# Performance work log

Hardware: AMD Instinct MI355X
Metric: run time of the kernel (lower is better)

## Reference

```python
import jax, jax.numpy as jnp
import numpy as np

N_LAYERS = 8
DILATIONS = [1, 2, 1, 2, 1, 2, 1, 2]
K_HOPS = 3
BN = 13248   # batch(64) * n_nodes(207), merged as in the torch module
L = 13       # 12 history steps + 1; shrinks by sum(dilations)=12 across layers
E = 211968   # BN * avg_degree(16)


def _conv1d(x, w, b, dil):
    # x: (BN, Cin, L), w: (Cout, Cin, 2) kernel-2 dilated conv, VALID (causal shrink)
    y = jax.lax.conv_general_dilated(x, w, (1,), 'VALID', rhs_dilation=(dil,),
                                     dimension_numbers=('NCH', 'OIH', 'NCH'))
    return y + b[None, :, None]


def setup_inputs() -> dict:
    key = jax.random.key(0)
    ks = jax.random.split(key, 20)
    s = 0.1  # keep activations in a sane range
    return {
        'x': jax.random.normal(ks[0], (BN, L, 2), jnp.float32),
        'edge_src': jax.random.randint(ks[1], (E,), 0, BN),
        'edge_dst': jax.random.randint(ks[2], (E,), 0, BN),
        'edge_w': jax.random.uniform(ks[3], (E,), jnp.float32),
        'init_w': s * jax.random.normal(ks[4], (2, 32), jnp.float32),
        'init_b': s * jax.random.normal(ks[5], (32,), jnp.float32),
        'filt_w': s * jax.random.normal(ks[6], (8, 32, 32, 2), jnp.float32),
        'filt_b': s * jax.random.normal(ks[7], (8, 32), jnp.float32),
        'gate_w': s * jax.random.normal(ks[8], (8, 32, 32, 2), jnp.float32),
        'gate_b': s * jax.random.normal(ks[9], (8, 32), jnp.float32),
        'gcn_w': s * jax.random.normal(ks[10], (8, 6, 32, 32), jnp.float32),
        'gcn_b': s * jax.random.normal(ks[11], (8, 32), jnp.float32),
        'skip_w': s * jax.random.normal(ks[12], (8, 256, 32), jnp.float32),
        'skip_b': s * jax.random.normal(ks[13], (8, 256), jnp.float32),
        'out0_w': s * jax.random.normal(ks[14], (256, 512), jnp.float32),
        'out0_b': s * jax.random.normal(ks[15], (512,), jnp.float32),
        'out1_w': s * jax.random.normal(ks[16], (512, 12), jnp.float32),
        'out1_b': s * jax.random.normal(ks[17], (12,), jnp.float32),
    }


def reference(x, edge_src, edge_dst, edge_w, init_w, init_b,
              filt_w, filt_b, gate_w, gate_b, gcn_w, gcn_b,
              skip_w, skip_b, out0_w, out0_b, out1_w, out1_b):
    # init linear: (BN, L, 2) -> (BN, L, 32) -> (BN, 32, L)
    h = (x @ init_w + init_b).transpose(0, 2, 1)
    # per-hop edge weights: elementwise powers of the transition weights
    # (faithful to repo's dense_to_sparse(transition ** k)); bck = transposed edges
    adjs = [(edge_src, edge_dst, edge_w ** k) for k in range(1, K_HOPS + 1)] + \
           [(edge_dst, edge_src, edge_w ** k) for k in range(1, K_HOPS + 1)]
    skip = None
    for l in range(N_LAYERS):
        d = DILATIONS[l]
        res = h
        # Gated TCN: tanh(filter) * sigmoid(gate), seq shrinks by d
        t = jnp.tanh(_conv1d(h, filt_w[l], filt_b[l], d)) * \
            jax.nn.sigmoid(_conv1d(h, gate_w[l], gate_b[l], d))
        # Diffusion conv: sum over 6 adjacency types of A_w (x W_a)
        xt = t.transpose(0, 2, 1)  # (BN, L', 32)
        g = jnp.zeros_like(xt)
        for a, (src, dst, w) in enumerate(adjs):
            msg = (xt @ gcn_w[l, a])[src] * w[:, None, None]  # (E, L', 32)
            g = g + jax.ops.segment_sum(msg, dst, num_segments=BN)
        h = g.transpose(0, 2, 1) + gcn_b[l][None, :, None]  # (BN, 32, L')
        # residual connection (align shrunk sequence)
        h = h + res[:, :, -h.shape[-1]:]
        # skip conv (1x1) on last timestep, accumulated
        sc = h[:, :, -1] @ skip_w[l].T + skip_b[l]  # (BN, 256)
        skip = sc if skip is None else skip + sc
    out = jax.nn.relu(skip)
    out = jax.nn.relu(out @ out0_w + out0_b)
    return out @ out1_w + out1_b  # (BN, 12)
```

## Files before the change

### kernel.cpp

```cpp
#include <hip/hip_runtime.h>
#include <hip/hip_fp16.h>

#define BN 13248
#define NE 211968
#define NBKT 8
#define SCAN_TOT (BN * NBKT)
#define SCAN_NBLK 52
#define ZSTRIDE 200
#define HSTRIDE 40
#define HNODE 480

typedef __attribute__((ext_vector_type(8))) short bf16x8;
typedef __attribute__((ext_vector_type(8))) _Float16 f16x8;
typedef __attribute__((ext_vector_type(4))) float f32x4;

__device__ __forceinline__ f32x4 mfma16b(bf16x8 a, bf16x8 b, f32x4 c) {
  return __builtin_amdgcn_mfma_f32_16x16x32_bf16(a, b, c, 0, 0, 0);
}
__device__ __forceinline__ f32x4 mfma16h(f16x8 a, f16x8 b, f32x4 c) {
  return __builtin_amdgcn_mfma_f32_16x16x32_f16(a, b, c, 0, 0, 0);
}

__device__ __forceinline__ unsigned short to_bf16(float v) {
  unsigned bits = __float_as_uint(v);
  return (unsigned short)((bits + 0x7FFFu + ((bits >> 16) & 1u)) >> 16);
}
__device__ __forceinline__ unsigned short to_f16(float v) {
  union { __half h; unsigned short s; } u; u.h = __float2half(v); return u.s;
}
__device__ __forceinline__ unsigned h2u(__half2 h) {
  union { __half2 h; unsigned u; } v; v.h = h; return v.u;
}
__device__ __forceinline__ __half2 u2h(unsigned u) {
  union { unsigned u; __half2 h; } v; v.u = u; return v.h;
}

__device__ __forceinline__ float fast_tanh(float x) {
  float e2 = __expf(2.f * x);
  return 1.f - 2.f / (e2 + 1.f);
}
__device__ __forceinline__ float fast_sig(float x) {
  return 1.f / (1.f + __expf(-x));
}

__global__ void k_count(const int* __restrict__ src, const int* __restrict__ dst,
                        int* __restrict__ cur_f, int* __restrict__ cur_b) {
  int e = blockIdx.x * 256 + threadIdx.x;
  if (e < NE) {
    int s = src[e], t = dst[e];
    atomicAdd(&cur_f[t * NBKT + (s >> 11)], 1);
    atomicAdd(&cur_b[s * NBKT + (t >> 11)], 1);
  }
}

__global__ __launch_bounds__(1024) void k_scan1(int* __restrict__ cnt_f, int* __restrict__ cnt_b,
                                                int* __restrict__ bsum) {
  __shared__ int sdata[1024];
  int b = blockIdx.x;
  int dir = (b >= SCAN_NBLK) ? 1 : 0;
  int lb = dir ? b - SCAN_NBLK : b;
  int* cnt = dir ? cnt_b : cnt_f;
  int tid = threadIdx.x;
  int i0 = lb * 2048 + tid * 2;
  int v0 = (i0 < SCAN_TOT) ? cnt[i0] : 0;
  int v1 = (i0 + 1 < SCAN_TOT) ? cnt[i0 + 1] : 0;
  int tot = v0 + v1;
  sdata[tid] = tot;
  __syncthreads();
  for (int off = 1; off < 1024; off <<= 1) {
    int add = (tid >= off) ? sdata[tid - off] : 0;
    __syncthreads();
    sdata[tid] += add;
    __syncthreads();
  }
  int excl = sdata[tid] - tot;
  if (i0 < SCAN_TOT) cnt[i0] = excl;
  if (i0 + 1 < SCAN_TOT) cnt[i0 + 1] = excl + v0;
  if (tid == 1023) bsum[b] = sdata[1023];
}

__global__ void k_scan2(int* __restrict__ bsum) {
  __shared__ int sdata[128];
  int tid = threadIdx.x;
  int seg = (tid >= 64) ? 64 : 0;
  int src = (tid < 64) ? tid : tid - 64 + SCAN_NBLK;
  int valid = ((tid & 63) < SCAN_NBLK);
  int v = valid ? bsum[src] : 0;
  sdata[tid] = v;
  __syncthreads();
  for (int off = 1; off < 64; off <<= 1) {
    int add = (tid - off >= seg) ? sdata[tid - off] : 0;
    __syncthreads();
    sdata[tid] += add;
    __syncthreads();
  }
  if (valid) bsum[src] = sdata[tid] - v;
}

__global__ __launch_bounds__(1024) void k_scan3(int* __restrict__ cnt_f, int* __restrict__ cnt_b,
                                                const int* __restrict__ bsum,
                                                int* __restrict__ row_f, int* __restrict__ row_b) {
  int b = blockIdx.x;
  int dir = (b >= SCAN_NBLK) ? 1 : 0;
  int lb = dir ? b - SCAN_NBLK : b;
  int* cnt = dir ? cnt_b : cnt_f;
  int* row = dir ? row_b : row_f;
  int off = bsum[b];
  int tid = threadIdx.x;
#pragma unroll
  for (int k = 0; k < 2; ++k) {
    int idx = lb * 2048 + tid * 2 + k;
    if (idx < SCAN_TOT) {
      int v = cnt[idx] + off;
      cnt[idx] = v;
      if ((idx & (NBKT - 1)) == 0) row[idx / NBKT] = v;
    }
  }
  if (b == 0 && tid == 0) { row_f[BN] = NE; row_b[BN] = NE; }
}

__global__ void k_fill(const int* __restrict__ src, const int* __restrict__ dst,
                       const float* __restrict__ w,
                       int* __restrict__ cur_f, int4* __restrict__ ce_f,
                       int* __restrict__ cur_b, int4* __restrict__ ce_b) {
  int e = blockIdx.x * 256 + threadIdx.x;
  if (e < NE) {
    int s = src[e], t = dst[e];
    float wv = w[e];
    float w2 = wv * wv, w3 = w2 * wv;
    int u1 = (int)h2u(__float2half2_rn(wv));
    int u2 = (int)h2u(__float2half2_rn(w2));
    int u3 = (int)h2u(__float2half2_rn(w3));
    int p = atomicAdd(&cur_f[t * NBKT + (s >> 11)], 1); ce_f[p] = make_int4(s, u1, u2, u3);
    int q = atomicAdd(&cur_b[s * NBKT + (t >> 11)], 1); ce_b[q] = make_int4(t, u1, u2, u3);
  }
}

__global__ void k_init(const float* __restrict__ x, const float* __restrict__ iw,
                       const float* __restrict__ ib, float* __restrict__ h) {
  int idx = blockIdx.x * 256 + threadIdx.x;
  if (idx >= BN * 13 * 32) return;
  int c = idx & 31;
  int r = idx >> 5;
  int n = r % BN;
  int tau = r / BN;
  float x0 = x[(n * 13 + tau) * 2 + 0];
  float x1 = x[(n * 13 + tau) * 2 + 1];
  h[idx] = fmaf(x0, iw[c], fmaf(x1, iw[32 + c], ib[c]));
}

__global__ void k_pack(const float* __restrict__ skip_w, const float* __restrict__ skip_b,
                       const float* __restrict__ w0, const float* __restrict__ w1,
                       const float* __restrict__ gcn_w,
                       const float* __restrict__ filt_w, const float* __restrict__ gate_w,
                       unsigned short* __restrict__ SWb, unsigned short* __restrict__ W0T,
                       unsigned short* __restrict__ W1T, float* __restrict__ bsum,
                       unsigned short* __restrict__ Gg16, unsigned short* __restrict__ WTC) {
  int id = blockIdx.x * 256 + threadIdx.x;
  if (id < 65536) {
    int j = id >> 8, k = id & 255;
    SWb[id] = to_bf16(skip_w[((k >> 5) * 256 + j) * 32 + (k & 31)]);
  }
  if (id < 131072) {
    int jo = id >> 8, k = id & 255;
    W0T[id] = to_bf16(w0[k * 512 + jo]);
  }
  if (id < 8192) {
    int n = id >> 9, k = id & 511;
    W1T[id] = (n < 12) ? to_bf16(w1[k * 12 + n]) : (unsigned short)0;
  }
  if (id < 256) {
    float s = 0.f;
    for (int l = 0; l < 8; ++l) s += skip_b[l * 256 + id];
    bsum[id] = s;
  }
  if (id < 49152) {
    int l = id / 6144, rem = id % 6144;
    int co = rem / 192, k = rem % 192;
    int a = k >> 5, ci = k & 31;
    Gg16[id] = to_f16(gcn_w[((l * 6 + a) * 32 + ci) * 32 + co]);
  }
  if (id < 32768) {
    int l = id >> 12, rem = id & 4095;
    int g = rem >> 11, co = (rem >> 6) & 31, k = rem & 63;
    const float* srcw = (g ? gate_w : filt_w) + l * 2048;
    float v = (k < 32) ? srcw[(co * 32 + k) * 2 + 0] : srcw[(co * 32 + (k - 32)) * 2 + 1];
    WTC[id] = to_f16(v);
  }
}

template<int LIN, int D, int TPAD>
__global__ __launch_bounds__(256) void k_tcn(const float* __restrict__ h_in, unsigned short* __restrict__ t_out,
    const float* __restrict__ fw, const float* __restrict__ fb,
    const float* __restrict__ gw, const float* __restrict__ gb) {
  constexpr int LOUT = LIN - D;
  __shared__ __align__(16) float wq[32 * 32 * 4];
  __shared__ float hl[8][LIN * 32];
  int tid = threadIdx.x;
  for (int f = tid; f < 4096; f += 256) {
    int e = f & 3, co = (f >> 2) & 31, ci = f >> 7;
    const float* srcw = (e < 2) ? fw : gw;
    wq[f] = srcw[(co * 32 + ci) * 2 + (e & 1)];
  }
  int n0 = blockIdx.x * 8;
  for (int i = tid; i < 8 * LIN * 32; i += 256) {
    int c = i & 31, r = i >> 5;
    int nl = r / LIN, tau = r % LIN;
    hl[nl][tau * 32 + c] = h_in[(tau * BN + n0 + nl) * 32 + c];
  }
  __syncthreads();
  int nl = tid >> 5, co = tid & 31;
  int n = n0 + nl;
  float accf[LOUT], accg[LOUT];
  float fbv = fb[co], gbv = gb[co];
#pragma unroll
  for (int j = 0; j < LOUT; ++j) { accf[j] = fbv; accg[j] = gbv; }
#pragma unroll
  for (int ci = 0; ci < 32; ++ci) {
    float4 wv = *(const float4*)&wq[(ci * 32 + co) * 4];
    float xr[LIN];
#pragma unroll
    for (int t = 0; t < LIN; ++t) xr[t] = hl[nl][t * 32 + ci];
#pragma unroll
    for (int j = 0; j < LOUT; ++j) {
      accf[j] = fmaf(xr[j], wv.x, accf[j]);
      accf[j] = fmaf(xr[j + D], wv.y, accf[j]);
      accg[j] = fmaf(xr[j], wv.z, accg[j]);
      accg[j] = fmaf(xr[j + D], wv.w, accg[j]);
    }
  }
#pragma unroll
  for (int j = 0; j < TPAD; ++j) {
    unsigned short v = 0;
    if (j < LOUT) v = to_f16(fast_tanh(accf[j < LOUT ? j : 0]) * fast_sig(accg[j < LOUT ? j : 0]));
    t_out[(n * TPAD + j) * 32 + co] = v;
  }
}

template<int NT>
__device__ __forceinline__ void edge_fma3(const int4& c, const uint2 (&u)[NT], __half2* A) {
  __half2 wh0 = u2h((unsigned)c.y), wh1 = u2h((unsigned)c.z), wh2 = u2h((unsigned)c.w);
#pragma unroll
  for (int j = 0; j < NT; ++j) {
    __half2 v0 = u2h(u[j].x), v1 = u2h(u[j].y);
    A[(0 * NT + j) * 2 + 0] = __hfma2(wh0, v0, A[(0 * NT + j) * 2 + 0]);
    A[(0 * NT + j) * 2 + 1] = __hfma2(wh0, v1, A[(0 * NT + j) * 2 + 1]);
    A[(1 * NT + j) * 2 + 0] = __hfma2(wh1, v0, A[(1 * NT + j) * 2 + 0]);
    A[(1 * NT + j) * 2 + 1] = __hfma2(wh1, v1, A[(1 * NT + j) * 2 + 1]);
    A[(2 * NT + j) * 2 + 0] = __hfma2(wh2, v0, A[(2 * NT + j) * 2 + 0]);
    A[(2 * NT + j) * 2 + 1] = __hfma2(wh2, v1, A[(2 * NT + j) * 2 + 1]);
  }
}

template<int TPAD, int NT, int LOUTT>
__device__ __forceinline__ void gather_one(const unsigned short* __restrict__ t_in,
    int e0, int e1, const int4* __restrict__ ce, int rowoff0, int rowbase, __half2* A) {
  constexpr bool FULL = (LOUTT >= TPAD);
  constexpr int EB = (NT == 3) ? 3 : ((NT == 2) ? 4 : 6);
  int e = e0;
  for (; e + EB <= e1; e += EB) {
    int4 c[EB];
    uint2 u[EB][NT];
#pragma unroll
    for (int k = 0; k < EB; ++k) c[k] = ce[e + k];
#pragma unroll
    for (int k = 0; k < EB; ++k) {
      const unsigned short* p = t_in + c[k].x * (TPAD * 32) + rowoff0;
#pragma unroll
      for (int j = 0; j < NT; ++j)
        u[k][j] = (FULL || rowbase + j < LOUTT) ? *(const uint2*)(p + j * 32) : make_uint2(0u, 0u);
    }
    __builtin_amdgcn_sched_barrier(0);
#pragma unroll
    for (int k = 0; k < EB; ++k) edge_fma3<NT>(c[k], u[k], A);
  }
  for (; e < e1; ++e) {
    int4 c1 = ce[e];
    uint2 u1[NT];
    const unsigned short* p = t_in + c1.x * (TPAD * 32) + rowoff0;
#pragma unroll
    for (int j = 0; j < NT; ++j)
      u1[j] = (FULL || rowbase + j < LOUTT) ? *(const uint2*)(p + j * 32) : make_uint2(0u, 0u);
    edge_fma3<NT>(c1, u1, A);
  }
}

template<int LOUT, int D, int TPAD, int D2, int TPAD2, bool LAST>
__global__ __launch_bounds__(128, 8) void k_fused(
    const unsigned short* __restrict__ t_in,
    const float* __restrict__ h_in, float* __restrict__ h_out,
    float* __restrict__ lastcol, unsigned short* __restrict__ t_next,
    const int* __restrict__ row_f, const int4* __restrict__ ce_f,
    const int* __restrict__ row_b, const int4* __restrict__ ce_b,
    const unsigned short* __restrict__ Wg,
    const float* __restrict__ bias,
    const unsigned short* __restrict__ Wtc,
    const float* __restrict__ fbn, const float* __restrict__ gbn) {
  constexpr int NT = TPAD / 4;
  constexpr int LOUT2 = LAST ? 1 : (LOUT - D2);
  constexpr int ZROWS = (2 * TPAD + 15) & ~15;
  constexpr int SBYTES = ZROWS * ZSTRIDE * 2;
  __shared__ __align__(16) char smem[SBYTES];
  unsigned short* Zl = (unsigned short*)smem;
  unsigned short* hb16 = (unsigned short*)smem;
  int tid = threadIdx.x;
  int nl = tid >> 6;
  int lane = tid & 63;
  int dh = lane >> 5;
  int lane32 = lane & 31;
  int tl = lane32 >> 3;
  int c4 = (lane32 & 7) << 2;
  int n0 = blockIdx.x * 2;
  int n = n0 + nl;
  int rowbase = tl * NT;
  int rowoff0 = rowbase * 32 + c4;
  const int* rowp = dh ? row_b : row_f;
  const int4* ce  = dh ? ce_b : ce_f;
  int e0 = rowp[n], e1 = rowp[n + 1];
  __half2 acc[3 * NT * 2];
  __half2 zero = __float2half2_rn(0.f);
#pragma unroll
  for (int i = 0; i < 3 * NT * 2; ++i) acc[i] = zero;
  gather_one<TPAD, NT, LOUT>(t_in, e0, e1, ce, rowoff0, rowbase, acc);
#pragma unroll
  for (int j = 0; j < NT; ++j) {
    int m = nl * TPAD + rowbase + j;
#pragma unroll
    for (int a3 = 0; a3 < 3; ++a3) {
      uint2 v = make_uint2(h2u(acc[(a3 * NT + j) * 2 + 0]), h2u(acc[(a3 * NT + j) * 2 + 1]));
      *(uint2*)(&Zl[m * ZSTRIDE + (dh * 3 + a3) * 32 + c4]) = v;
    }
  }
  __syncthreads();
  int wave = nl;
  int m16 = lane & 15, q = lane >> 4;
  constexpr int UPW = ZROWS / 16;
  f32x4 dacc[UPW];
#pragma unroll
  for (int i = 0; i < UPW; ++i) {
    int u = wave * UPW + i;
    int mt = u >> 1, nt = u & 1;
    dacc[i] = (f32x4){0.f, 0.f, 0.f, 0.f};
#pragma unroll
    for (int ks = 0; ks < 6; ++ks) {
      f16x8 av = *(const f16x8*)(&Zl[(mt * 16 + m16) * ZSTRIDE + ks * 32 + q * 8]);
      f16x8 bv = *(const f16x8*)((const _Float16*)Wg + (nt * 16 + m16) * 192 + ks * 32 + q * 8);
      dacc[i] = mfma16h(av, bv, dacc[i]);
    }
  }
  __syncthreads();
#pragma unroll
  for (int i = 0; i < UPW; ++i) {
    int u = wave * UPW + i;
    int mt = u >> 1, nt = u & 1;
    int co = nt * 16 + m16;
    float bco = bias[co];
#pragma unroll
    for (int r = 0; r < 4; ++r) {
      int mm = mt * 16 + q * 4 + r;
      int node = mm / TPAD;
      int tau = mm % TPAD;
      if (mm < 2 * TPAD && tau < LOUT) {
        float rres = h_in[((tau + D) * BN + n0 + node) * 32 + co];
        float o = dacc[i][r] + bco + rres;
        h_out[(tau * BN + n0 + node) * 32 + co] = o;
        if (!LAST) hb16[node * HNODE + tau * HSTRIDE + co] = to_f16(o);
        if (tau == LOUT - 1) lastcol[(n0 + node) * 32 + co] = o;
      }
    }
  }
  if (!LAST) {
    __syncthreads();
#pragma unroll
    for (int i = 0; i < 2; ++i) {
      int u = wave * 2 + i;
      int node = u >> 1, ntc = u & 1;
      int co = ntc * 16 + m16;
      f32x4 df = (f32x4){0.f, 0.f, 0.f, 0.f};
      f32x4 dg = (f32x4){0.f, 0.f, 0.f, 0.f};
#pragma unroll
      for (int s = 0; s < 2; ++s) {
        f16x8 av = *(const f16x8*)(&hb16[node * HNODE + (m16 + s * D2) * HSTRIDE + q * 8]);
        f16x8 bvf = *(const f16x8*)((const _Float16*)Wtc + (0 * 32 + co) * 64 + s * 32 + q * 8);
        f16x8 bvg = *(const f16x8*)((const _Float16*)Wtc + (1 * 32 + co) * 64 + s * 32 + q * 8);
        df = mfma16h(av, bvf, df);
        dg = mfma16h(av, bvg, dg);
      }
      float fbv = fbn[co], gbv = gbn[co];
#pragma unroll
      for (int r = 0; r < 4; ++r) {
        int j = q * 4 + r;
        if (j < TPAD2) {
          unsigned short v = 0;
          if (j < LOUT2)
            v = to_f16(fast_tanh(df[r] + fbv) * fast_sig(dg[r] + gbv));
          t_next[((n0 + node) * TPAD2 + j) * 32 + co] = v;
        }
      }
    }
  }
}

__device__ __forceinline__ bf16x8 ldsA(const unsigned short* buf, int stride, int row, int ks, int q) {
  int unit = ks * 4 + q;
  int addr = row * stride + ((unit ^ (row & 7)) << 3);
  return *(const bf16x8*)(buf + addr);
}

__global__ __launch_bounds__(256) void k_final(const float* __restrict__ lastcol,
    const unsigned short* __restrict__ SWb, const unsigned short* __restrict__ W0T,
    const unsigned short* __restrict__ W1T, const float* __restrict__ bsum,
    const float* __restrict__ b0, const float* __restrict__ b1,
    float* __restrict__ out) {
  __shared__ __align__(16) unsigned short Z[32 * 256];
  __shared__ __align__(16) unsigned short H[32 * 512];
  int tid = threadIdx.x;
  int wave = tid >> 6, lane = tid & 63;
  int m16 = lane & 15, q = lane >> 4;
  int n0 = blockIdx.x * 32;
#pragma unroll
  for (int it = 0; it < 32; ++it) {
    int id = it * 256 + tid;
    int m = id >> 8, k = id & 255;
    float v = lastcol[((k >> 5) * BN + n0 + m) * 32 + (k & 31)];
    Z[m * 256 + (((k >> 3) ^ (m & 7)) << 3) + (k & 7)] = to_bf16(v);
  }
  __syncthreads();
  f32x4 acc1[2][4];
#pragma unroll
  for (int mt = 0; mt < 2; ++mt)
#pragma unroll
    for (int i = 0; i < 4; ++i) acc1[mt][i] = (f32x4){0.f, 0.f, 0.f, 0.f};
#pragma unroll
  for (int ks = 0; ks < 8; ++ks) {
    bf16x8 a0 = ldsA(Z, 256, m16, ks, q);
    bf16x8 a1 = ldsA(Z, 256, 16 + m16, ks, q);
#pragma unroll
    for (int i = 0; i < 4; ++i) {
      int j = (wave * 4 + i) * 16 + m16;
      bf16x8 b = *(const bf16x8*)(SWb + j * 256 + ks * 32 + q * 8);
      acc1[0][i] = mfma16b(a0, b, acc1[0][i]);
      acc1[1][i] = mfma16b(a1, b, acc1[1][i]);
    }
  }
  __syncthreads();
#pragma unroll
  for (int i = 0; i < 4; ++i) {
    int j = (wave * 4 + i) * 16 + m16;
    float bs = bsum[j];
#pragma unroll
    for (int mt = 0; mt < 2; ++mt)
#pragma unroll
      for (int r = 0; r < 4; ++r) {
        int row = mt * 16 + q * 4 + r;
        float v = fmaxf(acc1[mt][i][r] + bs, 0.f);
        Z[row * 256 + (((j >> 3) ^ (row & 7)) << 3) + (j & 7)] = to_bf16(v);
      }
  }
  __syncthreads();
  f32x4 acc2[2][8];
#pragma unroll
  for (int mt = 0; mt < 2; ++mt)
#pragma unroll
    for (int i = 0; i < 8; ++i) acc2[mt][i] = (f32x4){0.f, 0.f, 0.f, 0.f};
#pragma unroll
  for (int ks = 0; ks < 8; ++ks) {
    bf16x8 a0 = ldsA(Z, 256, m16, ks, q);
    bf16x8 a1 = ldsA(Z, 256, 16 + m16, ks, q);
#pragma unroll
    for (int i = 0; i < 8; ++i) {
      int jo = (wave * 8 + i) * 16 + m16;
      bf16x8 b = *(const bf16x8*)(W0T + jo * 256 + ks * 32 + q * 8);
      acc2[0][i] = mfma16b(a0, b, acc2[0][i]);
      acc2[1][i] = mfma16b(a1, b, acc2[1][i]);
    }
  }
#pragma unroll
  for (int i = 0; i < 8; ++i) {
    int jo = (wave * 8 + i) * 16 + m16;
    float b0v = b0[jo];
#pragma unroll
    for (int mt = 0; mt < 2; ++mt)
#pragma unroll
      for (int r = 0; r < 4; ++r) {
        int row = mt * 16 + q * 4 + r;
        float v = fmaxf(acc2[mt][i][r] + b0v, 0.f);
        H[row * 512 + (((jo >> 3) ^ (row & 7)) << 3) + (jo & 7)] = to_bf16(v);
      }
  }
  __syncthreads();
  if (wave < 2) {
    f32x4 acc3 = (f32x4){0.f, 0.f, 0.f, 0.f};
#pragma unroll
    for (int ks = 0; ks < 16; ++ks) {
      bf16x8 a = ldsA(H, 512, wave * 16 + m16, ks, q);
      bf16x8 b = *(const bf16x8*)(W1T + m16 * 512 + ks * 32 + q * 8);
      acc3 = mfma16b(a, b, acc3);
    }
    if (m16 < 12) {
      float bv = b1[m16];
#pragma unroll
      for (int r = 0; r < 4; ++r)
        out[(n0 + wave * 16 + q * 4 + r) * 12 + m16] = acc3[r] + bv;
    }
  }
}

extern "C" void kernel_launch(void* const* d_in, const int* in_sizes, int n_in,
                              void* d_out, int out_size, void* d_ws, size_t ws_size,
                              hipStream_t stream) {
  const float* x      = (const float*)d_in[0];
  const int*   esrc   = (const int*)d_in[1];
  const int*   edst   = (const int*)d_in[2];
  const float* ew     = (const float*)d_in[3];
  const float* init_w = (const float*)d_in[4];
  const float* init_b = (const float*)d_in[5];
  const float* filt_w = (const float*)d_in[6];
  const float* filt_b = (const float*)d_in[7];
  const float* gate_w = (const float*)d_in[8];
  const float* gate_b = (const float*)d_in[9];
  const float* gcn_w  = (const float*)d_in[10];
  const float* gcn_b  = (const float*)d_in[11];
  const float* skip_w = (const float*)d_in[12];
  const float* skip_b = (const float*)d_in[13];
  const float* w0     = (const float*)d_in[14];
  const float* b0     = (const float*)d_in[15];
  const float* w1     = (const float*)d_in[16];
  const float* b1     = (const float*)d_in[17];
  float* out = (float*)d_out;

  float* base = (float*)d_ws;
  float* hA      = base;
  float* hB      = hA + 13 * BN * 32;
  unsigned short* tA = (unsigned short*)(hB + 13 * BN * 32);
  unsigned short* tB = tA + 12 * BN * 32;
  float* lastcol = (float*)(tB + 12 * BN * 32);
  int* row_f = (int*)(lastcol + 8 * BN * 32);
  int* row_b = row_f + (BN + 2);
  int* bscan = row_b + (BN + 2);
  int* cur_f = bscan + 128;
  int* cur_b = cur_f + BN * NBKT;
  int4* ce_f = (int4*)(cur_b + BN * NBKT);
  int4* ce_b = ce_f + NE;
  unsigned short* SWb  = (unsigned short*)(ce_b + NE);
  unsigned short* W0T  = SWb + 65536;
  unsigned short* W1T  = W0T + 131072;
  unsigned short* Gg16 = W1T + 8192;
  unsigned short* WTC  = Gg16 + 49152;
  float* bsumv = (float*)(WTC + 32768);

  hipMemsetAsync(cur_f, 0, 2 * BN * NBKT * sizeof(int), stream);
  const int egrid = (NE + 255) / 256;
  k_count<<<egrid, 256, 0, stream>>>(esrc, edst, cur_f, cur_b);
  k_scan1<<<2 * SCAN_NBLK, 1024, 0, stream>>>(cur_f, cur_b, bscan);
  k_scan2<<<1, 128, 0, stream>>>(bscan);
  k_scan3<<<2 * SCAN_NBLK, 1024, 0, stream>>>(cur_f, cur_b, bscan, row_f, row_b);
  k_fill<<<egrid, 256, 0, stream>>>(esrc, edst, ew, cur_f, ce_f, cur_b, ce_b);
  k_init<<<(BN * 13 * 32 + 255) / 256, 256, 0, stream>>>(x, init_w, init_b, hA);
  k_pack<<<512, 256, 0, stream>>>(skip_w, skip_b, w0, w1, gcn_w, filt_w, gate_w,
                                  SWb, W0T, W1T, bsumv, Gg16, WTC);

  k_tcn<13, 1, 12><<<BN / 8, 256, 0, stream>>>(hA, tA, filt_w, filt_b, gate_w, gate_b);

#define FUSED(l, LOUTv, Dv, TPv, D2v, TP2v, LASTv, tin, tout, hin, hout) \
  k_fused<LOUTv, Dv, TPv, D2v, TP2v, LASTv><<<BN / 2, 128, 0, stream>>>( \
      tin, hin, hout, lastcol + l * BN * 32, tout, row_f, ce_f, row_b, ce_b, \
      Gg16 + l * 6144, gcn_b + l * 32, WTC + (l + 1) * 4096, \
      filt_b + (l + 1) * 32, gate_b + (l + 1) * 32);

  FUSED(0, 12, 1, 12, 2, 12, false, tA, tB, hA, hB)
  FUSED(1, 10, 2, 12, 1, 12, false, tB, tA, hB, hA)
  FUSED(2,  9, 1, 12, 2,  8, false, tA, tB, hA, hB)
  FUSED(3,  7, 2,  8, 1,  8, false, tB, tA, hB, hA)
  FUSED(4,  6, 1,  8, 2,  4, false, tA, tB, hA, hB)
  FUSED(5,  4, 2,  4, 1,  4, false, tB, tA, hB, hA)
  FUSED(6,  3, 1,  4, 2,  4, false, tA, tB, hA, hB)
#undef FUSED
  k_fused<1, 2, 4, 2, 4, true><<<BN / 2, 128, 0, stream>>>(
      tB, hB, hA, lastcol + 7 * BN * 32, tA, row_f, ce_f, row_b, ce_b,
      Gg16 + 7 * 6144, gcn_b + 7 * 32, WTC, filt_b, gate_b);

  k_final<<<BN / 32, 256, 0, stream>>>(lastcol, SWb, W0T, W1T, bsumv, b0, b1, out);
}
```

Before: 655.1 us.

## Restructure fused GCN gather into one-node-per-wave async LDS staging pipeline

The fused layer kernel now runs one 64-lane wave per node instead of two nodes per 128-thread block. Each edge's neighbour row is streamed into LDS with global_load_lds through an 8-deep ring buffer, paced by explicit vmcnt waits, and the edge lists are staged into LDS in chunks. Forward and backward directions are handled sequentially within the wave. The goal is to keep more gather loads in flight and avoid register-staged uint2 loads. The cost is more LDS use per block, serialised directions, hand-written waitcnt logic and a changed MFMA tiling to one 16-row tile per node.

```diff
diff --git a/kernel.cpp b/kernel.cpp
--- a/kernel.cpp
+++ b/kernel.cpp
@@ -8,7 +8,6 @@
 #define SCAN_NBLK 52
 #define ZSTRIDE 200
 #define HSTRIDE 40
-#define HNODE 480
 
 typedef __attribute__((ext_vector_type(8))) short bf16x8;
 typedef __attribute__((ext_vector_type(8))) _Float16 f16x8;
@@ -41,6 +40,48 @@
 }
 __device__ __forceinline__ float fast_sig(float x) {
   return 1.f / (1.f + __expf(-x));
+}
+
+template<int N>
+__device__ __forceinline__ void vmwait() {
+  if constexpr (N == 0)       asm volatile("s_waitcnt vmcnt(0)" ::: "memory");
+  else if constexpr (N == 7)  asm volatile("s_waitcnt vmcnt(7)" ::: "memory");
+  else if constexpr (N == 14) asm volatile("s_waitcnt vmcnt(14)" ::: "memory");
+  else if constexpr (N == 21) asm volatile("s_waitcnt vmcnt(21)" ::: "memory");
+  __builtin_amdgcn_sched_barrier(0);
+}
+
+template<int NJ>
+__device__ __forceinline__ void stage_edge(const unsigned short* t_in, int node,
+                                           char* stg, int slot, int lane) {
+  const char* g = (const char*)t_in + (size_t)node * (NJ * 256);
+  char* l = stg + slot * (NJ * 256);
+#pragma unroll
+  for (int j = 0; j < NJ; ++j)
+    __builtin_amdgcn_global_load_lds(
+        (const __attribute__((address_space(1))) void*)(g + j * 256 + lane * 4),
+        (__attribute__((address_space(3))) void*)(l + j * 256), 4, 0, 0);
+}
+
+__device__ __forceinline__ void stage_ce(const int4* ce, int4* celds, int g, int lane) {
+  __builtin_amdgcn_global_load_lds(
+      (const __attribute__((address_space(1))) void*)(ce + g * 64 + lane),
+      (__attribute__((address_space(3))) void*)(celds + g * 64), 16, 0, 0);
+}
+
+template<int NJ>
+__device__ __forceinline__ void consume_edge(const char* stg, int slot,
+                                             const int4* celds, int i, int lane, __half2* A) {
+  int4 cw = celds[i];
+  __half2 w1 = u2h((unsigned)cw.y), w2 = u2h((unsigned)cw.z), w3 = u2h((unsigned)cw.w);
+  const char* sp = stg + slot * (NJ * 256);
+#pragma unroll
+  for (int j = 0; j < NJ; ++j) {
+    __half2 v = *(const __half2*)(sp + (j * 64 + lane) * 4);
+    A[0 * NJ + j] = __hfma2(w1, v, A[0 * NJ + j]);
+    A[1 * NJ + j] = __hfma2(w2, v, A[1 * NJ + j]);
+    A[2 * NJ + j] = __hfma2(w3, v, A[2 * NJ + j]);
+  }
 }
 
 __global__ void k_count(const int* __restrict__ src, const int* __restrict__ dst,
@@ -237,56 +278,8 @@
   }
 }
 
-template<int NT>
-__device__ __forceinline__ void edge_fma3(const int4& c, const uint2 (&u)[NT], __half2* A) {
-  __half2 wh0 = u2h((unsigned)c.y), wh1 = u2h((unsigned)c.z), wh2 = u2h((unsigned)c.w);
-#pragma unroll
-  for (int j = 0; j < NT; ++j) {
-    __half2 v0 = u2h(u[j].x), v1 = u2h(u[j].y);
-    A[(0 * NT + j) * 2 + 0] = __hfma2(wh0, v0, A[(0 * NT + j) * 2 + 0]);
-    A[(0 * NT + j) * 2 + 1] = __hfma2(wh0, v1, A[(0 * NT + j) * 2 + 1]);
-    A[(1 * NT + j) * 2 + 0] = __hfma2(wh1, v0, A[(1 * NT + j) * 2 + 0]);
-    A[(1 * NT + j) * 2 + 1] = __hfma2(wh1, v1, A[(1 * NT + j) * 2 + 1]);
-    A[(2 * NT + j) * 2 + 0] = __hfma2(wh2, v0, A[(2 * NT + j) * 2 + 0]);
-    A[(2 * NT + j) * 2 + 1] = __hfma2(wh2, v1, A[(2 * NT + j) * 2 + 1]);
-  }
-}
-
-template<int TPAD, int NT, int LOUTT>
-__device__ __forceinline__ void gather_one(const unsigned short* __restrict__ t_in,
-    int e0, int e1, const int4* __restrict__ ce, int rowoff0, int rowbase, __half2* A) {
-  constexpr bool FULL = (LOUTT >= TPAD);
-  constexpr int EB = (NT == 3) ? 3 : ((NT == 2) ? 4 : 6);
-  int e = e0;
-  for (; e + EB <= e1; e += EB) {
-    int4 c[EB];
-    uint2 u[EB][NT];
-#pragma unroll
-    for (int k = 0; k < EB; ++k) c[k] = ce[e + k];
-#pragma unroll
-    for (int k = 0; k < EB; ++k) {
-      const unsigned short* p = t_in + c[k].x * (TPAD * 32) + rowoff0;
-#pragma unroll
-      for (int j = 0; j < NT; ++j)
-        u[k][j] = (FULL || rowbase + j < LOUTT) ? *(const uint2*)(p + j * 32) : make_uint2(0u, 0u);
-    }
-    __builtin_amdgcn_sched_barrier(0);
-#pragma unroll
-    for (int k = 0; k < EB; ++k) edge_fma3<NT>(c[k], u[k], A);
-  }
-  for (; e < e1; ++e) {
-    int4 c1 = ce[e];
-    uint2 u1[NT];
-    const unsigned short* p = t_in + c1.x * (TPAD * 32) + rowoff0;
-#pragma unroll
-    for (int j = 0; j < NT; ++j)
-      u1[j] = (FULL || rowbase + j < LOUTT) ? *(const uint2*)(p + j * 32) : make_uint2(0u, 0u);
-    edge_fma3<NT>(c1, u1, A);
-  }
-}
-
 template<int LOUT, int D, int TPAD, int D2, int TPAD2, bool LAST>
-__global__ __launch_bounds__(128, 8) void k_fused(
+__global__ __launch_bounds__(64, 6) void k_fused(
     const unsigned short* __restrict__ t_in,
     const float* __restrict__ h_in, float* __restrict__ h_out,
     float* __restrict__ lastcol, unsigned short* __restrict__ t_next,
@@ -296,76 +289,99 @@
     const float* __restrict__ bias,
     const unsigned short* __restrict__ Wtc,
     const float* __restrict__ fbn, const float* __restrict__ gbn) {
-  constexpr int NT = TPAD / 4;
+  constexpr int NJ = TPAD / 4;
   constexpr int LOUT2 = LAST ? 1 : (LOUT - D2);
-  constexpr int ZROWS = (2 * TPAD + 15) & ~15;
-  constexpr int SBYTES = ZROWS * ZSTRIDE * 2;
-  __shared__ __align__(16) char smem[SBYTES];
+  constexpr int Q = 8;
+  constexpr int CAP = 128;
+  constexpr int BLKB = NJ * 256;
+  constexpr int STAGEB = Q * BLKB;
+  constexpr int GATB = STAGEB + CAP * 16;
+  constexpr int ZB = 16 * ZSTRIDE * 2;
+  constexpr int SBYTES = GATB > ZB ? GATB : ZB;
+  __shared__ __align__(256) char smem[SBYTES];
+  char* stg = smem;
+  int4* celds = (int4*)(smem + STAGEB);
   unsigned short* Zl = (unsigned short*)smem;
   unsigned short* hb16 = (unsigned short*)smem;
-  int tid = threadIdx.x;
-  int nl = tid >> 6;
-  int lane = tid & 63;
-  int dh = lane >> 5;
-  int lane32 = lane & 31;
-  int tl = lane32 >> 3;
-  int c4 = (lane32 & 7) << 2;
-  int n0 = blockIdx.x * 2;
-  int n = n0 + nl;
-  int rowbase = tl * NT;
-  int rowoff0 = rowbase * 32 + c4;
-  const int* rowp = dh ? row_b : row_f;
-  const int4* ce  = dh ? ce_b : ce_f;
-  int e0 = rowp[n], e1 = rowp[n + 1];
-  __half2 acc[3 * NT * 2];
+  int lane = threadIdx.x;
+  int n = blockIdx.x;
+  __half2 acc[6 * NJ];
   __half2 zero = __float2half2_rn(0.f);
 #pragma unroll
-  for (int i = 0; i < 3 * NT * 2; ++i) acc[i] = zero;
-  gather_one<TPAD, NT, LOUT>(t_in, e0, e1, ce, rowoff0, rowbase, acc);
-#pragma unroll
-  for (int j = 0; j < NT; ++j) {
-    int m = nl * TPAD + rowbase + j;
-#pragma unroll
-    for (int a3 = 0; a3 < 3; ++a3) {
-      uint2 v = make_uint2(h2u(acc[(a3 * NT + j) * 2 + 0]), h2u(acc[(a3 * NT + j) * 2 + 1]));
-      *(uint2*)(&Zl[m * ZSTRIDE + (dh * 3 + a3) * 32 + c4]) = v;
-    }
-  }
-  __syncthreads();
-  int wave = nl;
-  int m16 = lane & 15, q = lane >> 4;
-  constexpr int UPW = ZROWS / 16;
-  f32x4 dacc[UPW];
-#pragma unroll
-  for (int i = 0; i < UPW; ++i) {
-    int u = wave * UPW + i;
-    int mt = u >> 1, nt = u & 1;
-    dacc[i] = (f32x4){0.f, 0.f, 0.f, 0.f};
+  for (int i = 0; i < 6 * NJ; ++i) acc[i] = zero;
+
+#pragma unroll
+  for (int dh = 0; dh < 2; ++dh) {
+    const int* rowp = dh ? row_b : row_f;
+    const int4* cebase = dh ? ce_b : ce_f;
+    __half2* A = acc + dh * 3 * NJ;
+    int e0 = rowp[n], e1 = rowp[n + 1];
+    for (int c0 = e0; c0 < e1; c0 += CAP) {
+      int cnt = min(e1 - c0, CAP);
+      const int4* ce = cebase + c0;
+      int ng = (cnt + 63) >> 6;
+      for (int g = 0; g < ng; ++g) stage_ce(ce, celds, g, lane);
+      vmwait<0>();
+      if (cnt > Q) {
+        int cols[Q];
+#pragma unroll
+        for (int k = 0; k < Q; ++k) cols[k] = celds[k].x;
+#pragma unroll
+        for (int k = 0; k < Q; ++k) stage_edge<NJ>(t_in, cols[k], stg, k, lane);
+        int body = cnt - Q;
+        for (int i = 0; i < body; ++i) {
+          int nxt = celds[i + Q].x;
+          vmwait<(Q - 1) * NJ>();
+          consume_edge<NJ>(stg, i & (Q - 1), celds, i, lane, A);
+          stage_edge<NJ>(t_in, nxt, stg, (i + Q) & (Q - 1), lane);
+        }
+        vmwait<0>();
+        for (int i = body; i < cnt; ++i)
+          consume_edge<NJ>(stg, i & (Q - 1), celds, i, lane, A);
+      } else {
+        for (int k = 0; k < cnt; ++k) stage_edge<NJ>(t_in, celds[k].x, stg, k, lane);
+        vmwait<0>();
+        for (int i = 0; i < cnt; ++i) consume_edge<NJ>(stg, i, celds, i, lane, A);
+      }
+    }
+  }
+
+#pragma unroll
+  for (int j = 0; j < NJ; ++j) {
+    int u = j * 64 + lane;
+    int row = u >> 4, cp = u & 15;
+#pragma unroll
+    for (int a3 = 0; a3 < 6; ++a3)
+      *(unsigned*)(&Zl[row * ZSTRIDE + a3 * 32 + cp * 2]) = h2u(acc[a3 * NJ + j]);
+  }
+  __syncthreads();
+
+  int m16 = lane & 15, qq = lane >> 4;
+  f32x4 dacc[2];
+#pragma unroll
+  for (int nt = 0; nt < 2; ++nt) {
+    dacc[nt] = (f32x4){0.f, 0.f, 0.f, 0.f};
 #pragma unroll
     for (int ks = 0; ks < 6; ++ks) {
-      f16x8 av = *(const f16x8*)(&Zl[(mt * 16 + m16) * ZSTRIDE + ks * 32 + q * 8]);
-      f16x8 bv = *(const f16x8*)((const _Float16*)Wg + (nt * 16 + m16) * 192 + ks * 32 + q * 8);
-      dacc[i] = mfma16h(av, bv, dacc[i]);
-    }
-  }
-  __syncthreads();
-#pragma unroll
-  for (int i = 0; i < UPW; ++i) {
-    int u = wave * UPW + i;
-    int mt = u >> 1, nt = u & 1;
+      f16x8 av = *(const f16x8*)(&Zl[m16 * ZSTRIDE + ks * 32 + qq * 8]);
+      f16x8 bv = *(const f16x8*)((const _Float16*)Wg + (nt * 16 + m16) * 192 + ks * 32 + qq * 8);
+      dacc[nt] = mfma16h(av, bv, dacc[nt]);
+    }
+  }
+  __syncthreads();
+#pragma unroll
+  for (int nt = 0; nt < 2; ++nt) {
     int co = nt * 16 + m16;
     float bco = bias[co];
 #pragma unroll
     for (int r = 0; r < 4; ++r) {
-      int mm = mt * 16 + q * 4 + r;
-      int node = mm / TPAD;
-      int tau = mm % TPAD;
-      if (mm < 2 * TPAD && tau < LOUT) {
-        float rres = h_in[((tau + D) * BN + n0 + node) * 32 + co];
-        float o = dacc[i][r] + bco + rres;
-        h_out[(tau * BN + n0 + node) * 32 + co] = o;
-        if (!LAST) hb16[node * HNODE + tau * HSTRIDE + co] = to_f16(o);
-        if (tau == LOUT - 1) lastcol[(n0 + node) * 32 + co] = o;
+      int tau = qq * 4 + r;
+      if (tau < LOUT) {
+        float rres = h_in[((tau + D) * BN + n) * 32 + co];
+        float o = dacc[nt][r] + bco + rres;
+        h_out[(tau * BN + n) * 32 + co] = o;
+        if (!LAST) hb16[tau * HSTRIDE + co] = to_f16(o);
+        if (tau == LOUT - 1) lastcol[n * 32 + co] = o;
       }
     }
   }
@@ -373,28 +389,26 @@
     __syncthreads();
 #pragma unroll
     for (int i = 0; i < 2; ++i) {
-      int u = wave * 2 + i;
-      int node = u >> 1, ntc = u & 1;
-      int co = ntc * 16 + m16;
+      int co = i * 16 + m16;
       f32x4 df = (f32x4){0.f, 0.f, 0.f, 0.f};
       f32x4 dg = (f32x4){0.f, 0.f, 0.f, 0.f};
 #pragma unroll
       for (int s = 0; s < 2; ++s) {
-        f16x8 av = *(const f16x8*)(&hb16[node * HNODE + (m16 + s * D2) * HSTRIDE + q * 8]);
-        f16x8 bvf = *(const f16x8*)((const _Float16*)Wtc + (0 * 32 + co) * 64 + s * 32 + q * 8);
-        f16x8 bvg = *(const f16x8*)((const _Float16*)Wtc + (1 * 32 + co) * 64 + s * 32 + q * 8);
+        f16x8 av = *(const f16x8*)(&hb16[(m16 + s * D2) * HSTRIDE + qq * 8]);
+        f16x8 bvf = *(const f16x8*)((const _Float16*)Wtc + (0 * 32 + co) * 64 + s * 32 + qq * 8);
+        f16x8 bvg = *(const f16x8*)((const _Float16*)Wtc + (1 * 32 + co) * 64 + s * 32 + qq * 8);
         df = mfma16h(av, bvf, df);
         dg = mfma16h(av, bvg, dg);
       }
       float fbv = fbn[co], gbv = gbn[co];
 #pragma unroll
       for (int r = 0; r < 4; ++r) {
-        int j = q * 4 + r;
+        int j = qq * 4 + r;
         if (j < TPAD2) {
           unsigned short v = 0;
           if (j < LOUT2)
             v = to_f16(fast_tanh(df[r] + fbv) * fast_sig(dg[r] + gbv));
-          t_next[((n0 + node) * TPAD2 + j) * 32 + co] = v;
+          t_next[(n * TPAD2 + j) * 32 + co] = v;
         }
       }
     }
@@ -563,7 +577,7 @@
   k_tcn<13, 1, 12><<<BN / 8, 256, 0, stream>>>(hA, tA, filt_w, filt_b, gate_w, gate_b);
 
 #define FUSED(l, LOUTv, Dv, TPv, D2v, TP2v, LASTv, tin, tout, hin, hout) \
-  k_fused<LOUTv, Dv, TPv, D2v, TP2v, LASTv><<<BN / 2, 128, 0, stream>>>( \
+  k_fused<LOUTv, Dv, TPv, D2v, TP2v, LASTv><<<BN, 64, 0, stream>>>( \
       tin, hin, hout, lastcol + l * BN * 32, tout, row_f, ce_f, row_b, ce_b, \
       Gg16 + l * 6144, gcn_b + l * 32, WTC + (l + 1) * 4096, \
       filt_b + (l + 1) * 32, gate_b + (l + 1) * 32);
@@ -576,7 +590,7 @@
   FUSED(5,  4, 2,  4, 1,  4, false, tB, tA, hB, hA)
   FUSED(6,  3, 1,  4, 2,  4, false, tA, tB, hA, hB)
 #undef FUSED
-  k_fused<1, 2, 4, 2, 4, true><<<BN / 2, 128, 0, stream>>>(
+  k_fused<1, 2, 4, 2, 4, true><<<BN, 64, 0, stream>>>(
       tB, hB, hA, lastcol + 7 * BN * 32, tA, row_f, ce_f, row_b, ce_b,
       Gg16 + 7 * 6144, gcn_b + 7 * 32, WTC, filt_b, gate_b);
 
```

Measured after the change: 686.0 us. +4.7%, slower.
